# Kernel optimization log

Measured on AMD Instinct MI355X. Metric: run time of the kernel, lower is better.

The kernel has to match this reference:

```python
import jax, jax.numpy as jnp
import numpy as np

T = 8
TAU = 2.0       # spikingjelly LIFNode default tau
VTH = 1.0       # default v_threshold
ALPHA = 2.0     # surrogate.ATan alpha
EPS = 1e-5      # BatchNorm eps


@jax.custom_vjp
def spike_fn(x):
    # Heaviside with ATan surrogate gradient
    return (x >= 0.0).astype(x.dtype)

def _spike_fwd(x):
    return (x >= 0.0).astype(x.dtype), x

def _spike_bwd(x, g):
    sg = (ALPHA / 2.0) / (1.0 + (jnp.pi / 2.0 * ALPHA * x) ** 2)
    return (g * sg,)

spike_fn.defvjp(_spike_fwd, _spike_bwd)


def lif(x_seq):
    """Multi-step LIF over leading time axis. decay_input=True, hard reset to 0, detach_reset."""
    def step(v, x):
        v = v + (x - v) / TAU            # charge
        s = spike_fn(v - VTH)            # fire (surrogate grad)
        v = v * (1.0 - jax.lax.stop_gradient(s))  # detached hard reset to v_reset=0
        return v, s
    _, s_seq = jax.lax.scan(step, jnp.zeros_like(x_seq[0]), x_seq)
    return s_seq


def conv2d(x, w, b, stride):
    y = jax.lax.conv_general_dilated(x, w, (stride, stride), 'VALID',
                                     dimension_numbers=('NCHW', 'OIHW', 'NCHW'))
    return y + b[None, :, None, None]


def batchnorm(x, g, b):
    # training-mode BN over merged (T*B, H, W) axes, matching step_mode='m' BatchNorm2d
    m = x.mean((0, 2, 3), keepdims=True)
    v = x.var((0, 2, 3), keepdims=True)
    return g[None, :, None, None] * (x - m) * jax.lax.rsqrt(v + EPS) + b[None, :, None, None]


def setup_inputs() -> dict:
    key = jax.random.key(0)
    ks = jax.random.split(key, 12)
    def w_init(k, shape):
        fan_in = int(np.prod(shape[1:]))
        return jax.random.normal(k, shape, dtype=jnp.float32) / np.sqrt(fan_in)
    x = jax.random.normal(ks[0], (128, 4, 84, 84), dtype=jnp.float32)
    return {
        'x': x,
        'conv1_w': w_init(ks[1], (32, 4, 8, 8)),  'conv1_b': jnp.zeros((32,), jnp.float32),
        'bn1_g': jnp.ones((32,), jnp.float32),    'bn1_b': jnp.zeros((32,), jnp.float32),
        'conv2_w': w_init(ks[2], (64, 32, 4, 4)), 'conv2_b': jnp.zeros((64,), jnp.float32),
        'bn2_g': jnp.ones((64,), jnp.float32),    'bn2_b': jnp.zeros((64,), jnp.float32),
        'conv3_w': w_init(ks[3], (64, 64, 3, 3)), 'conv3_b': jnp.zeros((64,), jnp.float32),
        'bn3_g': jnp.ones((64,), jnp.float32),    'bn3_b': jnp.zeros((64,), jnp.float32),
        'fc1_w': w_init(ks[4], (512, 3136)),      'fc1_b': jnp.zeros((512,), jnp.float32),
        'fco_w': w_init(ks[5], (2, 512)),         'fco_b': jnp.zeros((2,), jnp.float32),
    }


def reference(x, conv1_w, conv1_b, bn1_g, bn1_b, conv2_w, conv2_b, bn2_g, bn2_b,
              conv3_w, conv3_b, bn3_g, bn3_b, fc1_w, fc1_b, fco_w, fco_b):
    B = x.shape[0]
    # replicate input over T timesteps; fold T into batch for conv/BN (step_mode='m')
    xs = jnp.broadcast_to(x, (T,) + x.shape).reshape((T * B,) + x.shape[1:])

    h = batchnorm(conv2d(xs, conv1_w, conv1_b, 4), bn1_g, bn1_b)   # [TB,32,20,20]
    s = lif(h.reshape((T, B) + h.shape[1:]))
    h = s.reshape((T * B,) + s.shape[2:])

    h = batchnorm(conv2d(h, conv2_w, conv2_b, 2), bn2_g, bn2_b)    # [TB,64,9,9]
    s = lif(h.reshape((T, B) + h.shape[1:]))
    h = s.reshape((T * B,) + s.shape[2:])

    h = batchnorm(conv2d(h, conv3_w, conv3_b, 1), bn3_g, bn3_b)    # [TB,64,7,7]
    s = lif(h.reshape((T, B) + h.shape[1:]))                        # [T,B,64,7,7]

    feat = s.reshape(T, B, -1)                                      # [T,B,3136]
    hid = lif(jnp.einsum('tbi,oi->tbo', feat, fc1_w) + fc1_b)       # [T,B,512]
    out_seq = jnp.einsum('tbo,ko->tbk', hid, fco_w) + fco_b         # [T,B,2]
    return out_seq.mean(0)                                          # [B,2]
```

## Files before the change

### kernel.cpp

```cpp
#include <hip/hip_runtime.h>
#include <cstdint>
#include <cstddef>

#define TT 8

#define E2_ELEMS (128*64*81)
#define E3_ELEMS (128*64*49)

typedef __attribute__((ext_vector_type(8))) short short8;
typedef __attribute__((ext_vector_type(4))) short short4v;
typedef __attribute__((ext_vector_type(4))) float f32x4;

#define BAR_LDS() do { asm volatile("s_waitcnt lgkmcnt(0)" ::: "memory"); \
                       __builtin_amdgcn_s_barrier(); } while (0)

__device__ __forceinline__ void gld_lds16(const void* g, void* l) {
  __builtin_amdgcn_global_load_lds((const __attribute__((address_space(1))) void*)g,
                                   (__attribute__((address_space(3))) void*)l, 16, 0, 0);
}

__device__ __forceinline__ void split3(float v, ushort& h, ushort& m, ushort& l) {
  union { __bf16 b; ushort u; } H, M, L;
  H.b = (__bf16)v; float r1 = v - (float)H.b;
  M.b = (__bf16)r1; float r2 = r1 - (float)M.b;
  L.b = (__bf16)r2;
  h = H.u; m = M.u; l = L.u;
}

__device__ __forceinline__ short8 ld8(const ushort* p) {
  union { short4v h[2]; short8 v; } U;
  U.h[0] = *(const short4v*)(p);
  U.h[1] = *(const short4v*)(p + 4);
  return U.v;
}

__global__ __launch_bounds__(256) void prep_all(const float* __restrict__ w1,
                                                const float* __restrict__ w2,
                                                const float* __restrict__ w3,
                                                const float* __restrict__ wfc,
                                                __bf16* __restrict__ w1f,
                                                __bf16* __restrict__ w2f,
                                                __bf16* __restrict__ w3f,
                                                __bf16* __restrict__ wff) {
  __shared__ float tile[12544];
  int bxx = blockIdx.x;
  int tid = threadIdx.x;

  if (bxx >= 912) {
    int bx2 = bxx - 912;
    int oc0 = (bx2 >> 3) * 32;
    int ci0 = (bx2 & 7) * 8;
    for (int f = tid; f < 12544; f += 256) {
      int oc_l = f / 392, r = f - oc_l * 392;
      tile[f] = wfc[(size_t)(oc0 + oc_l) * 3136 + ci0 * 49 + r];
    }
    __syncthreads();
    int squad = (ci0 & 31) >> 3;
    int sadd  = ci0 >> 5;
    for (int g = tid; g < 1568; g += 256) {
      int pos = g >> 5, oc_l = g & 31;
      union { __bf16 h[8]; uint4 u; } T0, T1, T2;
      #pragma unroll
      for (int j = 0; j < 8; j++) {
        float wv = tile[oc_l * 392 + j * 49 + pos];
        float hf = (float)(__bf16)wv;
        float r1 = wv - hf;
        float mf = (float)(__bf16)r1;
        float r2 = r1 - mf;
        T0.h[j] = (__bf16)wv; T1.h[j] = (__bf16)r1; T2.h[j] = (__bf16)r2;
      }
      int s = pos * 2 + sadd;
      size_t b0 = (((size_t)s * 4 + squad) * 512 + oc0 + oc_l) * 8;
      *(uint4*)(wff + b0)           = T0.u;
      *(uint4*)(wff + b0 + 1605632) = T1.u;
      *(uint4*)(wff + b0 + 3211264) = T2.u;
    }
    return;
  }

  int i = bxx * 256 + tid;
  if (i < 98304) {
    int v = i;
    int j    = v & 7;
    int oc   = (v >> 3) & 63;
    int quad = (v >> 9) & 3;
    int ksg  = (v >> 11) & 15;
    int term = v >> 15;
    int k = ksg * 32 + quad * 8 + j;
    int ci = k >> 4, kpos = k & 15;
    float w = w2[oc * 512 + ci * 16 + kpos];
    float hf = (float)(__bf16)w;
    float r1 = w - hf;
    float mf = (float)(__bf16)r1;
    float r2 = r1 - mf;
    w2f[v] = (term == 0) ? (__bf16)w : (term == 1) ? (__bf16)r1 : (__bf16)r2;
  } else if (i < 208896) {
    int v = i - 98304;
    int j    = v & 7;
    int oc   = (v >> 3) & 63;
    int quad = (v >> 9) & 3;
    int tk   = v >> 11;
    int term = tk / 18, kstep = tk % 18;
    int k = kstep * 32 + quad * 8 + j;
    int pos = k >> 6, ci = k & 63;
    float w = w3[oc * 576 + ci * 9 + pos];
    float hf = (float)(__bf16)w;
    float r1 = w - hf;
    float mf = (float)(__bf16)r1;
    float r2 = r1 - mf;
    w3f[v] = (term == 0) ? (__bf16)w : (term == 1) ? (__bf16)r1 : (__bf16)r2;
  } else {
    int v = i - 208896;
    int j    = v & 7;
    int oc   = (v >> 3) & 31;
    int quad = (v >> 8) & 3;
    int ks   = (v >> 10) & 7;
    int term = v >> 13;
    int k = ks * 32 + quad * 8 + j;
    float w = w1[oc * 256 + k];
    float hf = (float)(__bf16)w;
    float r1 = w - hf;
    float mf = (float)(__bf16)r1;
    float r2 = r1 - mf;
    w1f[v] = (term == 0) ? (__bf16)w : (term == 1) ? (__bf16)r1 : (__bf16)r2;
  }
}

__global__ __launch_bounds__(128) void k_conv1m(const float* __restrict__ x,
                                                const __bf16* __restrict__ w1f,
                                                const float* __restrict__ bias,
                                                float* __restrict__ out,
                                                float* __restrict__ pout) {
  __shared__ ushort xs[24192];
  int tid = threadIdx.x;
  int bx = blockIdx.x;
  int img = bx >> 2, q = bx & 3;
  const float* xb = x + (size_t)img * 28224 + q * 1680;
  for (int f = tid; f < 2016; f += 128) {
    int ci = f / 504, rr = f - ci * 504;
    int row = rr / 21, c4 = rr - row * 21;
    float4 v4 = *(const float4*)(xb + ci * 7056 + row * 84 + c4 * 4);
    union { ushort s[4]; uint2 u; } H, M, L;
    float vv[4] = {v4.x, v4.y, v4.z, v4.w};
    #pragma unroll
    for (int j = 0; j < 4; j++) split3(vv[j], H.s[j], M.s[j], L.s[j]);
    int eo = ci * 2016 + row * 84 + c4 * 4;
    *(uint2*)(xs + eo)         = H.u;
    *(uint2*)(xs + 8064 + eo)  = M.u;
    *(uint2*)(xs + 16128 + eo) = L.u;
  }
  __syncthreads();
  int nh = tid >> 6, lane = tid & 63;
  int l15 = lane & 15, quad = lane >> 4;
  int aoff[7];
  #pragma unroll
  for (int mt = 0; mt < 7; mt++) {
    int px = mt * 16 + l15; if (px > 99) px = 99;
    int oy = px / 20, ox = px - oy * 20;
    aoff[mt] = oy * 336 + ox * 4;
  }
  f32x4 acc[7];
  #pragma unroll
  for (int mt = 0; mt < 7; mt++) acc[mt] = (f32x4){0.f, 0.f, 0.f, 0.f};
  const __bf16* wpb = w1f + quad * 256 + (nh * 16 + l15) * 8;
  for (int ks = 0; ks < 8; ks++) {
    const __bf16* wp = wpb + ks * 1024;
    short8 bh = *(const short8*)(wp);
    short8 bm = *(const short8*)(wp + 8192);
    short8 bl = *(const short8*)(wp + 16384);
    int pair = ks * 4 + quad;
    int e0 = (pair >> 3) * 2016 + (pair & 7) * 84;
    short8 ah[7], am[7], al[7];
    #pragma unroll
    for (int mt = 0; mt < 7; mt++) {
      int e = e0 + aoff[mt];
      ah[mt] = ld8(xs + e);
      am[mt] = ld8(xs + 8064 + e);
      al[mt] = ld8(xs + 16128 + e);
    }
    #pragma unroll
    for (int mt = 0; mt < 7; mt++)
      acc[mt] = __builtin_amdgcn_mfma_f32_16x16x32_bf16(ah[mt], bh, acc[mt], 0, 0, 0);
    #pragma unroll
    for (int mt = 0; mt < 7; mt++)
      acc[mt] = __builtin_amdgcn_mfma_f32_16x16x32_bf16(ah[mt], bm, acc[mt], 0, 0, 0);
    #pragma unroll
    for (int mt = 0; mt < 7; mt++)
      acc[mt] = __builtin_amdgcn_mfma_f32_16x16x32_bf16(am[mt], bh, acc[mt], 0, 0, 0);
    #pragma unroll
    for (int mt = 0; mt < 7; mt++)
      acc[mt] = __builtin_amdgcn_mfma_f32_16x16x32_bf16(am[mt], bm, acc[mt], 0, 0, 0);
    #pragma unroll
    for (int mt = 0; mt < 7; mt++)
      acc[mt] = __builtin_amdgcn_mfma_f32_16x16x32_bf16(ah[mt], bl, acc[mt], 0, 0, 0);
    #pragma unroll
    for (int mt = 0; mt < 7; mt++)
      acc[mt] = __builtin_amdgcn_mfma_f32_16x16x32_bf16(al[mt], bh, acc[mt], 0, 0, 0);
    #pragma unroll
    for (int mt = 0; mt < 7; mt++)
      acc[mt] = __builtin_amdgcn_mfma_f32_16x16x32_bf16(am[mt], bl, acc[mt], 0, 0, 0);
    #pragma unroll
    for (int mt = 0; mt < 7; mt++)
      acc[mt] = __builtin_amdgcn_mfma_f32_16x16x32_bf16(al[mt], bm, acc[mt], 0, 0, 0);
  }
  int oc = nh * 16 + l15;
  float bv = bias[oc];
  float sl = 0.f, sl2 = 0.f;
  float* op = out + (size_t)img * 12800 + oc * 400 + q * 100;
  #pragma unroll
  for (int mt = 0; mt < 7; mt++) {
    int pxb = mt * 16 + quad * 4;
    #pragma unroll
    for (int r = 0; r < 4; r++) {
      int px = pxb + r;
      if (px < 100) {
        float v = acc[mt][r] + bv;
        op[px] = v;
        sl += v; sl2 += v * v;
      }
    }
  }
  __syncthreads();
  float* sred = (float*)xs;
  sred[oc * 4 + quad] = sl;
  sred[128 + oc * 4 + quad] = sl2;
  __syncthreads();
  if (tid < 32) {
    float s  = sred[tid*4] + sred[tid*4+1] + sred[tid*4+2] + sred[tid*4+3];
    float s2 = sred[128+tid*4] + sred[128+tid*4+1] + sred[128+tid*4+2] + sred[128+tid*4+3];
    pout[tid * 512 + bx] = s;
    pout[16384 + tid * 512 + bx] = s2;
  }
}

__global__ void k_bnfinal2(const float* __restrict__ pin, int sqoff, float n,
                           float* __restrict__ meanArr, float* __restrict__ rstdArr) {
  __shared__ float l0[256], l1[256];
  int c = blockIdx.x, tid = threadIdx.x;
  l0[tid] = pin[c * 512 + tid] + pin[c * 512 + tid + 256];
  l1[tid] = pin[sqoff + c * 512 + tid] + pin[sqoff + c * 512 + tid + 256];
  __syncthreads();
  for (int k = 128; k > 0; k >>= 1) {
    if (tid < k) { l0[tid] += l0[tid + k]; l1[tid] += l1[tid + k]; }
    __syncthreads();
  }
  if (tid == 0) {
    float m = l0[0] / n;
    float var = l1[0] / n - m * m;
    meanArr[c] = m;
    rstdArr[c] = rsqrtf(var + 1e-5f);
  }
}

__global__ void k_lif1b(const float* __restrict__ h, const float* __restrict__ mean,
                        const float* __restrict__ rstd, const float* __restrict__ g,
                        const float* __restrict__ bb, uint32_t* __restrict__ sout) {
  int idx = blockIdx.x * 256 + threadIdx.x;
  int ic = idx / 20;
  int ci = ic & 31;
  const float* hp = h + (size_t)idx * 20;
  float gm = g[ci], mm = mean[ci], rs = rstd[ci], bc = bb[ci];
  float xv[20];
  #pragma unroll
  for (int j4 = 0; j4 < 5; j4++) {
    float4 hv = ((const float4*)hp)[j4];
    xv[j4 * 4 + 0] = gm * (hv.x - mm) * rs + bc;
    xv[j4 * 4 + 1] = gm * (hv.y - mm) * rs + bc;
    xv[j4 * 4 + 2] = gm * (hv.z - mm) * rs + bc;
    xv[j4 * 4 + 3] = gm * (hv.w - mm) * rs + bc;
  }
  float v[20];
  #pragma unroll
  for (int j = 0; j < 20; j++) v[j] = 0.f;
  #pragma unroll
  for (int t = 0; t < TT; t++) {
    uint32_t w = 0;
    #pragma unroll
    for (int j = 0; j < 20; j++) {
      v[j] = v[j] + (xv[j] - v[j]) * 0.5f;
      uint32_t s = (v[j] >= 1.0f);
      w |= s << j;
      if (s) v[j] = 0.f;
    }
    sout[t * 81920 + idx] = w;
  }
}

__global__ __launch_bounds__(256) void k_conv2m(const uint32_t* __restrict__ s1b,
                                                const __bf16* __restrict__ wf,
                                                const float* __restrict__ bias,
                                                float* __restrict__ out,
                                                float* __restrict__ pout) {
  __shared__ uint32_t sp[1280];
  __shared__ uint4 wl4[3072];
  __bf16* wl = (__bf16*)wl4;
  int tid = threadIdx.x;
  int img0 = blockIdx.x * 2;
  {
    const uint32_t* src = s1b + (size_t)img0 * 640;
    for (int i = tid; i < 1280; i += 256) sp[i] = src[i];
  }
  int wave = tid >> 6, lane = tid & 63;
  int img_local = wave >> 1;
  int nh = wave & 1;
  int l15 = lane & 15, quad = lane >> 4;
  int ci_off = quad >> 1;
  int kyp = (quad & 1) * 2;
  int spb[6], sh[6];
  #pragma unroll
  for (int mt = 0; mt < 6; mt++) {
    int px = mt * 16 + l15;
    if (px > 80) px = 80;
    int oy = px / 9, ox = px - oy * 9;
    sh[mt]  = ox * 2;
    spb[mt] = img_local * 640 + ci_off * 20 + oy * 2 + kyp;
  }
  f32x4 acc[6][2];
  #pragma unroll
  for (int mt = 0; mt < 6; mt++)
    #pragma unroll
    for (int nt = 0; nt < 2; nt++) acc[mt][nt] = (f32x4){0.f, 0.f, 0.f, 0.f};

  for (int kc = 0; kc < 4; kc++) {
    __syncthreads();
    for (int o = tid * 8; o < 24576; o += 2048) {
      int tk = o >> 11;
      int term = tk >> 2, ksl = tk & 3;
      const __bf16* src = wf + (((term * 16 + kc * 4 + ksl)) << 11) + (o & 2047);
      gld_lds16(src, wl + o);
    }
    __syncthreads();
    #pragma unroll
    for (int ks = 0; ks < 4; ks++) {
      int ksg = kc * 4 + ks;
      short8 a[6];
      #pragma unroll
      for (int mt = 0; mt < 6; mt++) {
        uint32_t w0 = sp[spb[mt] + ksg * 40];
        uint32_t w1 = sp[spb[mt] + ksg * 40 + 1];
        uint32_t n0 = (w0 >> sh[mt]) & 15u;
        uint32_t n1 = (w1 >> sh[mt]) & 15u;
        union { uint32_t u[4]; short8 v; } A;
        A.u[0] = ((n0 & 1u) ? 0x3F80u : 0u) | ((n0 & 2u) ? 0x3F800000u : 0u);
        A.u[1] = ((n0 & 4u) ? 0x3F80u : 0u) | ((n0 & 8u) ? 0x3F800000u : 0u);
        A.u[2] = ((n1 & 1u) ? 0x3F80u : 0u) | ((n1 & 2u) ? 0x3F800000u : 0u);
        A.u[3] = ((n1 & 4u) ? 0x3F80u : 0u) | ((n1 & 8u) ? 0x3F800000u : 0u);
        a[mt] = A.v;
      }
      #pragma unroll
      for (int term = 0; term < 3; term++) {
        int fb = ((term * 4 + ks) << 11) + (quad << 9);
        #pragma unroll
        for (int nt = 0; nt < 2; nt++) {
          short8 b = *(const short8*)(wl + fb + ((((nh << 1) | nt) << 4) + l15) * 8);
          #pragma unroll
          for (int mt = 0; mt < 6; mt++)
            acc[mt][nt] = __builtin_amdgcn_mfma_f32_16x16x32_bf16(a[mt], b, acc[mt][nt], 0, 0, 0);
        }
      }
    }
  }
  float sl[2], sl2[2];
  #pragma unroll
  for (int nt = 0; nt < 2; nt++) {
    sl[nt] = 0.f; sl2[nt] = 0.f;
    int oc = nh * 32 + nt * 16 + l15;
    float bv = bias[oc];
    float* op = out + ((size_t)(img0 + img_local) * 64 + oc) * 81;
    #pragma unroll
    for (int mt = 0; mt < 6; mt++) {
      int pxr = mt * 16 + quad * 4;
      #pragma unroll
      for (int r = 0; r < 4; r++) {
        int px = pxr + r;
        if (px < 81) {
          float v = acc[mt][nt][r] + bv;
          op[px] = v;
          sl[nt] += v; sl2[nt] += v * v;
        }
      }
    }
  }
  __syncthreads();
  float* sred = (float*)wl4;
  #pragma unroll
  for (int nt = 0; nt < 2; nt++) {
    int oc = nh * 32 + nt * 16 + l15;
    int idx = oc * 8 + img_local * 4 + quad;
    sred[idx] = sl[nt];
    sred[512 + idx] = sl2[nt];
  }
  __syncthreads();
  if (tid < 64) {
    float s = 0.f, s2 = 0.f;
    #pragma unroll
    for (int k = 0; k < 8; k++) { s += sred[tid * 8 + k]; s2 += sred[512 + tid * 8 + k]; }
    pout[tid * 512 + blockIdx.x] = s;
    pout[32768 + tid * 512 + blockIdx.x] = s2;
  }
}

__global__ __launch_bounds__(256) void k_lifb2T(const float* __restrict__ h,
                                                const float* __restrict__ mean,
                                                const float* __restrict__ rstd,
                                                const float* __restrict__ g,
                                                const float* __restrict__ bb,
                                                uint32_t* __restrict__ s2T) {
  __shared__ uint32_t sb[288];
  int b = blockIdx.x, half = blockIdx.y;
  int tid = threadIdx.x;
  int c1 = half * 32 + tid / 9, py1 = tid % 9;
  bool has2 = tid < 32;
  int r2 = tid + 256;
  int c2i = half * 32 + r2 / 9, py2 = r2 % 9;
  float gm1 = g[c1], mm1 = mean[c1], rs1 = rstd[c1], bc1 = bb[c1];
  float gm2 = 0.f, mm2 = 0.f, rs2 = 0.f, bc2 = 0.f;
  if (has2) { gm2 = g[c2i]; mm2 = mean[c2i]; rs2 = rstd[c2i]; bc2 = bb[c2i]; }
  float v1[9], v2[9];
  #pragma unroll
  for (int j = 0; j < 9; j++) { v1[j] = 0.f; v2[j] = 0.f; }
  size_t base1 = ((size_t)b * 64 + c1) * 81 + py1 * 9;
  size_t base2 = has2 ? ((size_t)b * 64 + c2i) * 81 + py2 * 9 : base1;
  float c1v[9], c2v[9];
  {
    const float* hp = h;
    #pragma unroll
    for (int j = 0; j < 9; j++) c1v[j] = hp[base1 + j];
    if (has2) {
      #pragma unroll
      for (int j = 0; j < 9; j++) c2v[j] = hp[base2 + j];
    }
  }
  #pragma unroll 1
  for (int t = 0; t < TT; t++) {
    float n1v[9], n2v[9];
    if (t < TT - 1) {
      const float* hp = h + (size_t)(t + 1) * E2_ELEMS;
      #pragma unroll
      for (int j = 0; j < 9; j++) n1v[j] = hp[base1 + j];
      if (has2) {
        #pragma unroll
        for (int j = 0; j < 9; j++) n2v[j] = hp[base2 + j];
      }
    }
    uint32_t w = 0;
    #pragma unroll
    for (int j = 0; j < 9; j++) {
      float xv = gm1 * (c1v[j] - mm1) * rs1 + bc1;
      v1[j] = v1[j] + (xv - v1[j]) * 0.5f;
      uint32_t s = (v1[j] >= 1.0f);
      w |= s << j;
      if (s) v1[j] = 0.f;
    }
    sb[tid] = w;
    if (has2) {
      uint32_t w2 = 0;
      #pragma unroll
      for (int j = 0; j < 9; j++) {
        float xv = gm2 * (c2v[j] - mm2) * rs2 + bc2;
        v2[j] = v2[j] + (xv - v2[j]) * 0.5f;
        uint32_t s = (v2[j] >= 1.0f);
        w2 |= s << j;
        if (s) v2[j] = 0.f;
      }
      sb[r2] = w2;
    }
    BAR_LDS();
    if (tid < 81) {
      int r = tid / 9, cpix = tid - r * 9;
      uint32_t wo = 0;
      #pragma unroll
      for (int ci = 0; ci < 32; ci++)
        wo |= ((sb[ci * 9 + r] >> cpix) & 1u) << ci;
      s2T[(size_t)(t * 128 + b) * 162 + tid * 2 + half] = wo;
    }
    BAR_LDS();
    if (t < TT - 1) {
      #pragma unroll
      for (int j = 0; j < 9; j++) c1v[j] = n1v[j];
      if (has2) {
        #pragma unroll
        for (int j = 0; j < 9; j++) c2v[j] = n2v[j];
      }
    }
  }
}

__global__ __launch_bounds__(256) void k_conv3m(const uint32_t* __restrict__ s2T,
                                                const __bf16* __restrict__ wf,
                                                const float* __restrict__ bias,
                                                float* __restrict__ out,
                                                float* __restrict__ pout) {
  __shared__ uint32_t sp[324];
  __shared__ uint4 wl4[4608];
  __bf16* wl = (__bf16*)wl4;
  int tid = threadIdx.x;
  int img0 = blockIdx.x * 2;
  {
    const uint32_t* src = s2T + (size_t)img0 * 162;
    for (int i = tid; i < 324; i += 256) sp[i] = src[i];
  }
  int wave = tid >> 6, lane = tid & 63;
  int img_local = wave >> 1, nh = wave & 1;
  int l15 = lane & 15, quad = lane >> 4;
  int qsh = quad * 8;
  int base[4];
  #pragma unroll
  for (int mt = 0; mt < 4; mt++) {
    int px = mt * 16 + l15;
    if (px > 48) px = 48;
    int oy = px / 7, ox = px - oy * 7;
    base[mt] = img_local * 162 + (oy * 9 + ox) * 2;
  }
  f32x4 acc[4][2];
  #pragma unroll
  for (int mt = 0; mt < 4; mt++)
    #pragma unroll
    for (int nt = 0; nt < 2; nt++) acc[mt][nt] = (f32x4){0.f, 0.f, 0.f, 0.f};

  #pragma unroll
  for (int kc = 0; kc < 3; kc++) {
    __syncthreads();
    #pragma unroll
    for (int it = 0; it < 18; it++) {
      const __bf16* s = wf + (((it / 6) * 18 + kc * 6 + (it % 6)) << 11) + tid * 8;
      gld_lds16(s, wl + (it << 11) + tid * 8);
    }
    __syncthreads();
    #pragma unroll
    for (int ksl = 0; ksl < 6; ksl++) {
      int kstep = kc * 6 + ksl;
      int pos = kstep >> 1, cihalf = kstep & 1;
      int ky = pos / 3, kx = pos % 3;
      short8 a[4];
      #pragma unroll
      for (int mt = 0; mt < 4; mt++) {
        uint32_t word = sp[base[mt] + (ky * 9 + kx) * 2 + cihalf];
        uint32_t byt = (word >> qsh) & 255u;
        union { uint32_t u[4]; short8 v; } A;
        A.u[0] = ((byt & 1u)  ? 0x3F80u : 0u) | ((byt & 2u)   ? 0x3F800000u : 0u);
        A.u[1] = ((byt & 4u)  ? 0x3F80u : 0u) | ((byt & 8u)   ? 0x3F800000u : 0u);
        A.u[2] = ((byt & 16u) ? 0x3F80u : 0u) | ((byt & 32u)  ? 0x3F800000u : 0u);
        A.u[3] = ((byt & 64u) ? 0x3F80u : 0u) | ((byt & 128u) ? 0x3F800000u : 0u);
        a[mt] = A.v;
      }
      #pragma unroll
      for (int term = 0; term < 3; term++) {
        int fb = ((term * 6 + ksl) << 11) + (quad << 9);
        #pragma unroll
        for (int nt = 0; nt < 2; nt++) {
          short8 b = *(const short8*)(wl + fb + ((((nh << 1) | nt) << 4) + l15) * 8);
          #pragma unroll
          for (int mt = 0; mt < 4; mt++)
            acc[mt][nt] = __builtin_amdgcn_mfma_f32_16x16x32_bf16(a[mt], b, acc[mt][nt], 0, 0, 0);
        }
      }
    }
  }
  float sl[2], sl2[2];
  #pragma unroll
  for (int nt = 0; nt < 2; nt++) {
    sl[nt] = 0.f; sl2[nt] = 0.f;
    int oc = nh * 32 + nt * 16 + l15;
    float bv = bias[oc];
    float* op = out + ((size_t)(img0 + img_local) * 64 + oc) * 49;
    #pragma unroll
    for (int mt = 0; mt < 4; mt++) {
      int pxr = mt * 16 + quad * 4;
      #pragma unroll
      for (int r = 0; r < 4; r++) {
        int px = pxr + r;
        if (px < 49) {
          float v = acc[mt][nt][r] + bv;
          op[px] = v;
          sl[nt] += v; sl2[nt] += v * v;
        }
      }
    }
  }
  __syncthreads();
  float* sred = (float*)wl4;
  #pragma unroll
  for (int nt = 0; nt < 2; nt++) {
    int oc = nh * 32 + nt * 16 + l15;
    int idx = oc * 8 + img_local * 4 + quad;
    sred[idx] = sl[nt];
    sred[512 + idx] = sl2[nt];
  }
  __syncthreads();
  if (tid < 64) {
    float s = 0.f, s2 = 0.f;
    #pragma unroll
    for (int k = 0; k < 8; k++) { s += sred[tid * 8 + k]; s2 += sred[512 + tid * 8 + k]; }
    pout[tid * 512 + blockIdx.x] = s;
    pout[32768 + tid * 512 + blockIdx.x] = s2;
  }
}

__global__ __launch_bounds__(256) void k_lifb3T(const float* __restrict__ h,
                                                const float* __restrict__ mean,
                                                const float* __restrict__ rstd,
                                                const float* __restrict__ g,
                                                const float* __restrict__ bb,
                                                uint32_t* __restrict__ s3T) {
  __shared__ uint32_t sb[224];
  int b = blockIdx.x, half = blockIdx.y;
  int tid = threadIdx.x;
  bool active = tid < 224;
  int row = active ? tid : 0;
  int c = half * 32 + row / 7, py = row % 7;
  float gm = g[c], mm = mean[c], rs = rstd[c], bc = bb[c];
  float v[7];
  #pragma unroll
  for (int j = 0; j < 7; j++) v[j] = 0.f;
  size_t base = ((size_t)b * 64 + c) * 49 + py * 7;
  float cv[7];
  if (active) {
    #pragma unroll
    for (int j = 0; j < 7; j++) cv[j] = h[base + j];
  }
  #pragma unroll 1
  for (int t = 0; t < TT; t++) {
    float nv[7];
    if (active && t < TT - 1) {
      const float* hp = h + (size_t)(t + 1) * E3_ELEMS;
      #pragma unroll
      for (int j = 0; j < 7; j++) nv[j] = hp[base + j];
    }
    if (active) {
      uint32_t w = 0;
      #pragma unroll
      for (int j = 0; j < 7; j++) {
        float xv = gm * (cv[j] - mm) * rs + bc;
        v[j] = v[j] + (xv - v[j]) * 0.5f;
        uint32_t s = (v[j] >= 1.0f);
        w |= s << j;
        if (s) v[j] = 0.f;
      }
      sb[tid] = w;
    }
    BAR_LDS();
    if (tid < 49) {
      int py2 = tid / 7, px = tid - py2 * 7;
      uint32_t wo = 0;
      #pragma unroll
      for (int ci = 0; ci < 32; ci++)
        wo |= ((sb[ci * 7 + py2] >> px) & 1u) << ci;
      s3T[(size_t)(t * 128 + b) * 98 + tid * 2 + half] = wo;
    }
    BAR_LDS();
    if (active && t < TT - 1) {
      #pragma unroll
      for (int j = 0; j < 7; j++) cv[j] = nv[j];
    }
  }
}

__global__ __launch_bounds__(256) void k_fc1m(const uint32_t* __restrict__ s3T,
                                              const __bf16* __restrict__ wf,
                                              float* __restrict__ f1) {
  __shared__ uint32_t aS[6272];
  int tid = threadIdx.x;
  int row0 = blockIdx.x * 64;
  int oc0  = blockIdx.y * 16;
  {
    const uint32_t* src = s3T + (size_t)row0 * 98;
    for (int i = tid; i < 6272; i += 256) aS[i] = src[i];
  }
  __syncthreads();
  int wave = tid >> 6, lane = tid & 63;
  int l15 = lane & 15, quad = lane >> 4;
  int qsh = quad * 8;
  f32x4 acc[4];
  #pragma unroll
  for (int mt = 0; mt < 4; mt++) acc[mt] = (f32x4){0.f, 0.f, 0.f, 0.f};
  int nIter = (wave < 2) ? 25 : 24;
  #pragma unroll 2
  for (int i = 0; i < nIter; i++) {
    int ks = i * 4 + wave;
    short8 a[4];
    #pragma unroll
    for (int mt = 0; mt < 4; mt++) {
      uint32_t word = aS[(mt * 16 + l15) * 98 + ks];
      uint32_t byt = (word >> qsh) & 255u;
      union { uint32_t u[4]; short8 v; } A;
      A.u[0] = ((byt & 1u)  ? 0x3F80u : 0u) | ((byt & 2u)   ? 0x3F800000u : 0u);
      A.u[1] = ((byt & 4u)  ? 0x3F80u : 0u) | ((byt & 8u)   ? 0x3F800000u : 0u);
      A.u[2] = ((byt & 16u) ? 0x3F80u : 0u) | ((byt & 32u)  ? 0x3F800000u : 0u);
      A.u[3] = ((byt & 64u) ? 0x3F80u : 0u) | ((byt & 128u) ? 0x3F800000u : 0u);
      a[mt] = A.v;
    }
    #pragma unroll
    for (int term = 0; term < 3; term++) {
      size_t fb = ((size_t)((term * 98 + ks) * 4 + quad) * 512 + oc0 + l15) * 8;
      short8 b = *(const short8*)(wf + fb);
      #pragma unroll
      for (int mt = 0; mt < 4; mt++)
        acc[mt] = __builtin_amdgcn_mfma_f32_16x16x32_bf16(a[mt], b, acc[mt], 0, 0, 0);
    }
  }
  __syncthreads();
  float* red = (float*)aS;
  #pragma unroll
  for (int mt = 0; mt < 4; mt++)
    #pragma unroll
    for (int r = 0; r < 4; r++)
      red[(wave * 64 + lane) * 17 + mt * 4 + r] = acc[mt][r];
  __syncthreads();
  #pragma unroll
  for (int k = 0; k < 4; k++) {
    int oi = tid + k * 256;
    int row_l = oi >> 4, oc_l = oi & 15;
    int mt = row_l >> 4, rem = row_l & 15;
    int q2 = rem >> 2, r = rem & 3;
    int ln = q2 * 16 + oc_l;
    float s = red[(0 * 64 + ln) * 17 + mt * 4 + r];
    s += red[(1 * 64 + ln) * 17 + mt * 4 + r];
    s += red[(2 * 64 + ln) * 17 + mt * 4 + r];
    s += red[(3 * 64 + ln) * 17 + mt * 4 + r];
    f1[(size_t)(row0 + row_l) * 512 + oc0 + oc_l] = s;
  }
}

__global__ __launch_bounds__(256) void k_fc1fco(const float* __restrict__ f1,
                                                const float* __restrict__ bias,
                                                const float* __restrict__ w,
                                                const float* __restrict__ fcob,
                                                float* __restrict__ out) {
  int b = blockIdx.x, tid = threadIdx.x;
  int o0 = tid, o1 = tid + 256;
  float bv0 = bias[o0], bv1 = bias[o1];
  float w00 = w[o0], w10 = w[512 + o0];
  float w01 = w[o1], w11 = w[512 + o1];
  float x0[TT], x1[TT];
  #pragma unroll
  for (int t = 0; t < TT; t++) {
    x0[t] = f1[(size_t)(t * 128 + b) * 512 + o0];
    x1[t] = f1[(size_t)(t * 128 + b) * 512 + o1];
  }
  float v0 = 0.f, v1 = 0.f;
  float a0 = 0.f, a1 = 0.f;
  #pragma unroll
  for (int t = 0; t < TT; t++) {
    float s0 = x0[t] + bv0;
    v0 = v0 + (s0 - v0) * 0.5f;
    bool sp0 = (v0 >= 1.0f);
    if (sp0) v0 = 0.f;
    float s1 = x1[t] + bv1;
    v1 = v1 + (s1 - v1) * 0.5f;
    bool sp1 = (v1 >= 1.0f);
    if (sp1) v1 = 0.f;
    if (sp0) { a0 += w00; a1 += w10; }
    if (sp1) { a0 += w01; a1 += w11; }
  }
  __shared__ float l0[256], l1[256];
  l0[tid] = a0; l1[tid] = a1; __syncthreads();
  for (int k = 128; k > 0; k >>= 1) {
    if (tid < k) { l0[tid] += l0[tid + k]; l1[tid] += l1[tid + k]; }
    __syncthreads();
  }
  if (tid == 0) {
    out[b * 2 + 0] = l0[0] * 0.125f + fcob[0];
    out[b * 2 + 1] = l1[0] * 0.125f + fcob[1];
  }
}

extern "C" void kernel_launch(void* const* d_in, const int* in_sizes, int n_in,
                              void* d_out, int out_size, void* d_ws, size_t ws_size,
                              hipStream_t stream) {
  const float* x    = (const float*)d_in[0];
  const float* c1w  = (const float*)d_in[1];
  const float* c1b  = (const float*)d_in[2];
  const float* bn1g = (const float*)d_in[3];
  const float* bn1b = (const float*)d_in[4];
  const float* c2w  = (const float*)d_in[5];
  const float* c2b  = (const float*)d_in[6];
  const float* bn2g = (const float*)d_in[7];
  const float* bn2b = (const float*)d_in[8];
  const float* c3w  = (const float*)d_in[9];
  const float* c3b  = (const float*)d_in[10];
  const float* bn3g = (const float*)d_in[11];
  const float* bn3b = (const float*)d_in[12];
  const float* fc1w = (const float*)d_in[13];
  const float* fc1b = (const float*)d_in[14];
  const float* fcow = (const float*)d_in[15];
  const float* fcob = (const float*)d_in[16];
  float* out = (float*)d_out;

  char* ws = (char*)d_ws;
  float*    h1     = (float*)(ws + 0);
  uint32_t* s1bits = (uint32_t*)(ws + 6553600);
  float*    h2     = (float*)(ws + 19660800);
  float*    h3     = (float*)(ws + 46202880);
  __bf16*   w2f    = (__bf16*)(ws + 60882944);
  __bf16*   w3f    = (__bf16*)(ws + 61079552);
  uint32_t* s2T    = (uint32_t*)(ws + 61300736);
  __bf16*   w1f    = (__bf16*)(ws + 62390272);
  float*    st     = (float*)(ws + 64880640);
  __bf16*   wff    = (__bf16*)(ws + 67108864);
  float*    f1sum  = (float*)(ws + 76742656);
  uint32_t* s3T    = (uint32_t*)(ws + 85131264);
  float*    bnpart = (float*)(ws + 85532672);

  prep_all   <<<1040, 256, 0, stream>>>(c1w, c2w, c3w, fc1w, w1f, w2f, w3f, wff);

  k_conv1m   <<<512, 128, 0, stream>>>(x, w1f, c1b, h1, bnpart);
  k_bnfinal2 <<<32, 256, 0, stream>>>(bnpart, 16384, 51200.f, st, st + 32);
  k_lif1b    <<<320, 256, 0, stream>>>(h1, st, st + 32, bn1g, bn1b, s1bits);

  k_conv2m   <<<512, 256, 0, stream>>>(s1bits, w2f, c2b, h2, bnpart);
  k_bnfinal2 <<<64, 256, 0, stream>>>(bnpart, 32768, 82944.f, st + 64, st + 128);
  k_lifb2T   <<<dim3(128, 2), 256, 0, stream>>>(h2, st + 64, st + 128, bn2g, bn2b, s2T);

  k_conv3m   <<<512, 256, 0, stream>>>(s2T, w3f, c3b, h3, bnpart);
  k_bnfinal2 <<<64, 256, 0, stream>>>(bnpart, 32768, 50176.f, st + 192, st + 256);
  k_lifb3T   <<<dim3(128, 2), 256, 0, stream>>>(h3, st + 192, st + 256, bn3g, bn3b, s3T);

  k_fc1m     <<<dim3(16, 32), 256, 0, stream>>>(s3T, wff, f1sum);
  k_fc1fco   <<<128, 256, 0, stream>>>(f1sum, fc1b, fcow, fcob, out);
}
```

Baseline: 233.0 us.

## Fuse BN finalization into consumers and LIF1 into conv2 input staging

Removes the three k_bnfinal2 launches: each consumer block now reduces the BN partial sums itself with wave shuffles and keeps mean/rstd in shared memory. It also removes k_lif1b and the s1bits buffer. conv2 recomputes layer-1 BN+LIF spike bits for its images directly from h1, re-running the LIF recurrence up to the block's timestep. This cuts kernel launches and one global round trip. The cost is redundant work: every block repeats the stats reduction, and the LIF recurrence is recomputed per timestep, up to 8 iterations with a data-dependent loop.

```diff
diff --git a/kernel.cpp b/kernel.cpp
--- a/kernel.cpp
+++ b/kernel.cpp
@@ -32,6 +32,34 @@
   U.h[0] = *(const short4v*)(p);
   U.h[1] = *(const short4v*)(p + 4);
   return U.v;
+}
+
+__device__ __forceinline__ void bn_wave_stats(const float* __restrict__ p0,
+                                              const float* __restrict__ p1,
+                                              int ln, float n,
+                                              float* __restrict__ stm,
+                                              float* __restrict__ str, int cl) {
+  float a0 = p0[ln]       + p0[ln + 256];
+  float a2 = p0[ln + 128] + p0[ln + 384];
+  float a1 = p0[ln + 64]  + p0[ln + 320];
+  float a3 = p0[ln + 192] + p0[ln + 448];
+  float s  = (a0 + a2) + (a1 + a3);
+  float q0 = p1[ln]       + p1[ln + 256];
+  float q2 = p1[ln + 128] + p1[ln + 384];
+  float q1 = p1[ln + 64]  + p1[ln + 320];
+  float q3 = p1[ln + 192] + p1[ln + 448];
+  float sq = (q0 + q2) + (q1 + q3);
+  #pragma unroll
+  for (int mask = 32; mask >= 1; mask >>= 1) {
+    s  += __shfl_xor(s,  mask);
+    sq += __shfl_xor(sq, mask);
+  }
+  if (ln == 0) {
+    float m = s / n;
+    float var = sq / n - m * m;
+    stm[cl] = m;
+    str[cl] = rsqrtf(var + 1e-5f);
+  }
 }
 
 __global__ __launch_bounds__(256) void prep_all(const float* __restrict__ w1,
@@ -233,73 +261,52 @@
   }
 }
 
-__global__ void k_bnfinal2(const float* __restrict__ pin, int sqoff, float n,
-                           float* __restrict__ meanArr, float* __restrict__ rstdArr) {
-  __shared__ float l0[256], l1[256];
-  int c = blockIdx.x, tid = threadIdx.x;
-  l0[tid] = pin[c * 512 + tid] + pin[c * 512 + tid + 256];
-  l1[tid] = pin[sqoff + c * 512 + tid] + pin[sqoff + c * 512 + tid + 256];
-  __syncthreads();
-  for (int k = 128; k > 0; k >>= 1) {
-    if (tid < k) { l0[tid] += l0[tid + k]; l1[tid] += l1[tid + k]; }
-    __syncthreads();
-  }
-  if (tid == 0) {
-    float m = l0[0] / n;
-    float var = l1[0] / n - m * m;
-    meanArr[c] = m;
-    rstdArr[c] = rsqrtf(var + 1e-5f);
-  }
-}
-
-__global__ void k_lif1b(const float* __restrict__ h, const float* __restrict__ mean,
-                        const float* __restrict__ rstd, const float* __restrict__ g,
-                        const float* __restrict__ bb, uint32_t* __restrict__ sout) {
-  int idx = blockIdx.x * 256 + threadIdx.x;
-  int ic = idx / 20;
-  int ci = ic & 31;
-  const float* hp = h + (size_t)idx * 20;
-  float gm = g[ci], mm = mean[ci], rs = rstd[ci], bc = bb[ci];
-  float xv[20];
-  #pragma unroll
-  for (int j4 = 0; j4 < 5; j4++) {
-    float4 hv = ((const float4*)hp)[j4];
-    xv[j4 * 4 + 0] = gm * (hv.x - mm) * rs + bc;
-    xv[j4 * 4 + 1] = gm * (hv.y - mm) * rs + bc;
-    xv[j4 * 4 + 2] = gm * (hv.z - mm) * rs + bc;
-    xv[j4 * 4 + 3] = gm * (hv.w - mm) * rs + bc;
-  }
-  float v[20];
-  #pragma unroll
-  for (int j = 0; j < 20; j++) v[j] = 0.f;
-  #pragma unroll
-  for (int t = 0; t < TT; t++) {
-    uint32_t w = 0;
-    #pragma unroll
-    for (int j = 0; j < 20; j++) {
-      v[j] = v[j] + (xv[j] - v[j]) * 0.5f;
-      uint32_t s = (v[j] >= 1.0f);
-      w |= s << j;
-      if (s) v[j] = 0.f;
-    }
-    sout[t * 81920 + idx] = w;
-  }
-}
-
-__global__ __launch_bounds__(256) void k_conv2m(const uint32_t* __restrict__ s1b,
+__global__ __launch_bounds__(256) void k_conv2m(const float* __restrict__ h1,
+                                                const float* __restrict__ bnp,
+                                                const float* __restrict__ g1,
+                                                const float* __restrict__ b1,
                                                 const __bf16* __restrict__ wf,
                                                 const float* __restrict__ bias,
                                                 float* __restrict__ out,
                                                 float* __restrict__ pout) {
   __shared__ uint32_t sp[1280];
   __shared__ uint4 wl4[3072];
+  __shared__ float stm[32], str[32];
   __bf16* wl = (__bf16*)wl4;
   int tid = threadIdx.x;
   int img0 = blockIdx.x * 2;
-  {
-    const uint32_t* src = s1b + (size_t)img0 * 640;
-    for (int i = tid; i < 1280; i += 256) sp[i] = src[i];
-  }
+  int t_blk = img0 >> 7;
+  int b0 = img0 & 127;
+  int wavei = tid >> 6, ln = tid & 63;
+  for (int c = wavei; c < 32; c += 4)
+    bn_wave_stats(bnp + c * 512, bnp + 16384 + c * 512, ln, 51200.f, stm, str, c);
+  __syncthreads();
+  for (int wi = tid; wi < 1280; wi += 256) {
+    int img_local = wi / 640, r = wi - img_local * 640;
+    int ci = (r / 20) & 31;
+    const float* hp = h1 + ((size_t)(b0 + img_local) * 640 + r) * 20;
+    float gm = g1[ci], mm = stm[ci], rs = str[ci], bc = b1[ci];
+    uint32_t w = 0;
+    #pragma unroll
+    for (int j4 = 0; j4 < 5; j4++) {
+      float4 hv = ((const float4*)hp)[j4];
+      float xsv[4] = {hv.x, hv.y, hv.z, hv.w};
+      #pragma unroll
+      for (int j = 0; j < 4; j++) {
+        float xv = gm * (xsv[j] - mm) * rs + bc;
+        float v = 0.f; uint32_t sbit = 0;
+        for (int tt = 0; tt <= t_blk; tt++) {
+          v = v + (xv - v) * 0.5f;
+          sbit = (v >= 1.0f);
+          if (sbit) v = 0.f;
+        }
+        w |= sbit << (j4 * 4 + j);
+      }
+    }
+    sp[wi] = w;
+  }
+  __syncthreads();
+
   int wave = tid >> 6, lane = tid & 63;
   int img_local = wave >> 1;
   int nh = wave & 1;
@@ -401,21 +408,27 @@
 }
 
 __global__ __launch_bounds__(256) void k_lifb2T(const float* __restrict__ h,
-                                                const float* __restrict__ mean,
-                                                const float* __restrict__ rstd,
+                                                const float* __restrict__ bnp,
                                                 const float* __restrict__ g,
                                                 const float* __restrict__ bb,
                                                 uint32_t* __restrict__ s2T) {
   __shared__ uint32_t sb[288];
+  __shared__ float stm[32], str[32];
   int b = blockIdx.x, half = blockIdx.y;
   int tid = threadIdx.x;
+  int wavei = tid >> 6, ln = tid & 63;
+  for (int cl = wavei; cl < 32; cl += 4) {
+    int c = half * 32 + cl;
+    bn_wave_stats(bnp + c * 512, bnp + 32768 + c * 512, ln, 82944.f, stm, str, cl);
+  }
+  __syncthreads();
   int c1 = half * 32 + tid / 9, py1 = tid % 9;
   bool has2 = tid < 32;
   int r2 = tid + 256;
   int c2i = half * 32 + r2 / 9, py2 = r2 % 9;
-  float gm1 = g[c1], mm1 = mean[c1], rs1 = rstd[c1], bc1 = bb[c1];
+  float gm1 = g[c1], mm1 = stm[tid / 9], rs1 = str[tid / 9], bc1 = bb[c1];
   float gm2 = 0.f, mm2 = 0.f, rs2 = 0.f, bc2 = 0.f;
-  if (has2) { gm2 = g[c2i]; mm2 = mean[c2i]; rs2 = rstd[c2i]; bc2 = bb[c2i]; }
+  if (has2) { gm2 = g[c2i]; mm2 = stm[r2 / 9]; rs2 = str[r2 / 9]; bc2 = bb[c2i]; }
   float v1[9], v2[9];
   #pragma unroll
   for (int j = 0; j < 9; j++) { v1[j] = 0.f; v2[j] = 0.f; }
@@ -598,18 +611,24 @@
 }
 
 __global__ __launch_bounds__(256) void k_lifb3T(const float* __restrict__ h,
-                                                const float* __restrict__ mean,
-                                                const float* __restrict__ rstd,
+                                                const float* __restrict__ bnp,
                                                 const float* __restrict__ g,
                                                 const float* __restrict__ bb,
                                                 uint32_t* __restrict__ s3T) {
   __shared__ uint32_t sb[224];
+  __shared__ float stm[32], str[32];
   int b = blockIdx.x, half = blockIdx.y;
   int tid = threadIdx.x;
+  int wavei = tid >> 6, ln = tid & 63;
+  for (int cl = wavei; cl < 32; cl += 4) {
+    int c = half * 32 + cl;
+    bn_wave_stats(bnp + c * 512, bnp + 32768 + c * 512, ln, 50176.f, stm, str, cl);
+  }
+  __syncthreads();
   bool active = tid < 224;
   int row = active ? tid : 0;
   int c = half * 32 + row / 7, py = row % 7;
-  float gm = g[c], mm = mean[c], rs = rstd[c], bc = bb[c];
+  float gm = g[c], mm = stm[row / 7], rs = str[row / 7], bc = bb[c];
   float v[7];
   #pragma unroll
   for (int j = 0; j < 7; j++) v[j] = 0.f;
@@ -789,33 +808,27 @@
 
   char* ws = (char*)d_ws;
   float*    h1     = (float*)(ws + 0);
-  uint32_t* s1bits = (uint32_t*)(ws + 6553600);
   float*    h2     = (float*)(ws + 19660800);
   float*    h3     = (float*)(ws + 46202880);
   __bf16*   w2f    = (__bf16*)(ws + 60882944);
   __bf16*   w3f    = (__bf16*)(ws + 61079552);
   uint32_t* s2T    = (uint32_t*)(ws + 61300736);
   __bf16*   w1f    = (__bf16*)(ws + 62390272);
-  float*    st     = (float*)(ws + 64880640);
   __bf16*   wff    = (__bf16*)(ws + 67108864);
   float*    f1sum  = (float*)(ws + 76742656);
   uint32_t* s3T    = (uint32_t*)(ws + 85131264);
-  float*    bnpart = (float*)(ws + 85532672);
-
-  prep_all   <<<1040, 256, 0, stream>>>(c1w, c2w, c3w, fc1w, w1f, w2f, w3f, wff);
-
-  k_conv1m   <<<512, 128, 0, stream>>>(x, w1f, c1b, h1, bnpart);
-  k_bnfinal2 <<<32, 256, 0, stream>>>(bnpart, 16384, 51200.f, st, st + 32);
-  k_lif1b    <<<320, 256, 0, stream>>>(h1, st, st + 32, bn1g, bn1b, s1bits);
-
-  k_conv2m   <<<512, 256, 0, stream>>>(s1bits, w2f, c2b, h2, bnpart);
-  k_bnfinal2 <<<64, 256, 0, stream>>>(bnpart, 32768, 82944.f, st + 64, st + 128);
-  k_lifb2T   <<<dim3(128, 2), 256, 0, stream>>>(h2, st + 64, st + 128, bn2g, bn2b, s2T);
-
-  k_conv3m   <<<512, 256, 0, stream>>>(s2T, w3f, c3b, h3, bnpart);
-  k_bnfinal2 <<<64, 256, 0, stream>>>(bnpart, 32768, 50176.f, st + 192, st + 256);
-  k_lifb3T   <<<dim3(128, 2), 256, 0, stream>>>(h3, st + 192, st + 256, bn3g, bn3b, s3T);
-
-  k_fc1m     <<<dim3(16, 32), 256, 0, stream>>>(s3T, wff, f1sum);
-  k_fc1fco   <<<128, 256, 0, stream>>>(f1sum, fc1b, fcow, fcob, out);
-}
+  float*    bnpA   = (float*)(ws + 85532672);
+  float*    bnpB   = (float*)(ws + 85794816);
+
+  prep_all <<<1040, 256, 0, stream>>>(c1w, c2w, c3w, fc1w, w1f, w2f, w3f, wff);
+
+  k_conv1m <<<512, 128, 0, stream>>>(x, w1f, c1b, h1, bnpA);
+  k_conv2m <<<512, 256, 0, stream>>>(h1, bnpA, bn1g, bn1b, w2f, c2b, h2, bnpB);
+  k_lifb2T <<<dim3(128, 2), 256, 0, stream>>>(h2, bnpB, bn2g, bn2b, s2T);
+
+  k_conv3m <<<512, 256, 0, stream>>>(s2T, w3f, c3b, h3, bnpB);
+  k_lifb3T <<<dim3(128, 2), 256, 0, stream>>>(h3, bnpB, bn3g, bn3b, s3T);
+
+  k_fc1m   <<<dim3(16, 32), 256, 0, stream>>>(s3T, wff, f1sum);
+  k_fc1fco <<<128, 256, 0, stream>>>(f1sum, fc1b, fcow, fcob, out);
+}
```

Measured after the change: 262.6 us. 1.13x slower.

## Split conv2/conv3 blocks by output-channel half and preload full weight slice

Applied to the files above, without the earlier changes.

Conv2 and conv3 blocks now each handle four images and one half of the output channels, instead of two images and all channels. Each block loads its whole weight slice into LDS once before the main loop, so the per-chunk reload and barriers inside the K loop go away. The partial-stat reduction is reindexed so the per-512 pout layout stays the same. LDS use per block grows a lot (about 100-115 KB), which may cut occupancy to one block per CU. The staged weight load is no longer overlapped with compute.

```diff
diff --git a/kernel.cpp b/kernel.cpp
--- a/kernel.cpp
+++ b/kernel.cpp
@@ -291,18 +291,31 @@
                                                 const float* __restrict__ bias,
                                                 float* __restrict__ out,
                                                 float* __restrict__ pout) {
-  __shared__ uint32_t sp[1280];
-  __shared__ uint4 wl4[3072];
+  __shared__ uint4 wl4[6144];
+  __shared__ uint32_t sp[2560];
+  __shared__ float sred[1024];
   __bf16* wl = (__bf16*)wl4;
   int tid = threadIdx.x;
-  int img0 = blockIdx.x * 2;
+  int bx = blockIdx.x;
+  int img_group = bx >> 1;
+  int nh = bx & 1;
   {
-    const uint32_t* src = s1b + (size_t)img0 * 640;
-    for (int i = tid; i < 1280; i += 256) sp[i] = src[i];
-  }
+    const uint32_t* src = s1b + (size_t)img_group * 2560;
+    for (int i = tid; i < 2560; i += 256) sp[i] = src[i];
+  }
+  #pragma unroll
+  for (int r = 0; r < 24; r++) {
+    int idx = r * 256 + tid;
+    int chunk = idx >> 5, ln32 = idx & 31;
+    int quad_c = chunk & 3, tq = chunk >> 2;
+    int term = tq % 3, ksg = tq / 3;
+    const __bf16* src = wf + term * 32768 + ksg * 2048 + quad_c * 512 + nh * 256 + ln32 * 8;
+    gld_lds16(src, wl + idx * 8);
+  }
+  __syncthreads();
+
   int wave = tid >> 6, lane = tid & 63;
-  int img_local = wave >> 1;
-  int nh = wave & 1;
+  int img = img_group * 4 + wave;
   int l15 = lane & 15, quad = lane >> 4;
   int ci_off = quad >> 1;
   int kyp = (quad & 1) * 2;
@@ -313,7 +326,7 @@
     if (px > 80) px = 80;
     int oy = px / 9, ox = px - oy * 9;
     sh[mt]  = ox * 2;
-    spb[mt] = img_local * 640 + ci_off * 20 + oy * 2 + kyp;
+    spb[mt] = wave * 640 + ci_off * 20 + oy * 2 + kyp;
   }
   f32x4 acc[6][2];
   #pragma unroll
@@ -321,42 +334,30 @@
     #pragma unroll
     for (int nt = 0; nt < 2; nt++) acc[mt][nt] = (f32x4){0.f, 0.f, 0.f, 0.f};
 
-  for (int kc = 0; kc < 4; kc++) {
-    __syncthreads();
-    for (int o = tid * 8; o < 24576; o += 2048) {
-      int tk = o >> 11;
-      int term = tk >> 2, ksl = tk & 3;
-      const __bf16* src = wf + (((term * 16 + kc * 4 + ksl)) << 11) + (o & 2047);
-      gld_lds16(src, wl + o);
-    }
-    __syncthreads();
-    #pragma unroll
-    for (int ks = 0; ks < 4; ks++) {
-      int ksg = kc * 4 + ks;
-      short8 a[6];
-      #pragma unroll
-      for (int mt = 0; mt < 6; mt++) {
-        uint32_t w0 = sp[spb[mt] + ksg * 40];
-        uint32_t w1 = sp[spb[mt] + ksg * 40 + 1];
-        uint32_t n0 = (w0 >> sh[mt]) & 15u;
-        uint32_t n1 = (w1 >> sh[mt]) & 15u;
-        union { uint32_t u[4]; short8 v; } A;
-        A.u[0] = ((n0 & 1u) ? 0x3F80u : 0u) | ((n0 & 2u) ? 0x3F800000u : 0u);
-        A.u[1] = ((n0 & 4u) ? 0x3F80u : 0u) | ((n0 & 8u) ? 0x3F800000u : 0u);
-        A.u[2] = ((n1 & 1u) ? 0x3F80u : 0u) | ((n1 & 2u) ? 0x3F800000u : 0u);
-        A.u[3] = ((n1 & 4u) ? 0x3F80u : 0u) | ((n1 & 8u) ? 0x3F800000u : 0u);
-        a[mt] = A.v;
-      }
-      #pragma unroll
-      for (int term = 0; term < 3; term++) {
-        int fb = ((term * 4 + ks) << 11) + (quad << 9);
+  #pragma unroll 2
+  for (int ksg = 0; ksg < 16; ksg++) {
+    short8 a[6];
+    #pragma unroll
+    for (int mt = 0; mt < 6; mt++) {
+      uint32_t w0 = sp[spb[mt] + ksg * 40];
+      uint32_t w1 = sp[spb[mt] + ksg * 40 + 1];
+      uint32_t n0 = (w0 >> sh[mt]) & 15u;
+      uint32_t n1 = (w1 >> sh[mt]) & 15u;
+      union { uint32_t u[4]; short8 v; } A;
+      A.u[0] = ((n0 & 1u) ? 0x3F80u : 0u) | ((n0 & 2u) ? 0x3F800000u : 0u);
+      A.u[1] = ((n0 & 4u) ? 0x3F80u : 0u) | ((n0 & 8u) ? 0x3F800000u : 0u);
+      A.u[2] = ((n1 & 1u) ? 0x3F80u : 0u) | ((n1 & 2u) ? 0x3F800000u : 0u);
+      A.u[3] = ((n1 & 4u) ? 0x3F80u : 0u) | ((n1 & 8u) ? 0x3F800000u : 0u);
+      a[mt] = A.v;
+    }
+    #pragma unroll
+    for (int term = 0; term < 3; term++) {
+      #pragma unroll
+      for (int nt = 0; nt < 2; nt++) {
+        short8 b = *(const short8*)(wl + (((ksg * 3 + term) * 4 + quad) << 8) + (nt * 16 + l15) * 8);
         #pragma unroll
-        for (int nt = 0; nt < 2; nt++) {
-          short8 b = *(const short8*)(wl + fb + ((((nh << 1) | nt) << 4) + l15) * 8);
-          #pragma unroll
-          for (int mt = 0; mt < 6; mt++)
-            acc[mt][nt] = __builtin_amdgcn_mfma_f32_16x16x32_bf16(a[mt], b, acc[mt][nt], 0, 0, 0);
-        }
+        for (int mt = 0; mt < 6; mt++)
+          acc[mt][nt] = __builtin_amdgcn_mfma_f32_16x16x32_bf16(a[mt], b, acc[mt][nt], 0, 0, 0);
       }
     }
   }
@@ -364,9 +365,10 @@
   #pragma unroll
   for (int nt = 0; nt < 2; nt++) {
     sl[nt] = 0.f; sl2[nt] = 0.f;
-    int oc = nh * 32 + nt * 16 + l15;
+    int ocl = nt * 16 + l15;
+    int oc = nh * 32 + ocl;
     float bv = bias[oc];
-    float* op = out + ((size_t)(img0 + img_local) * 64 + oc) * 81;
+    float* op = out + ((size_t)img * 64 + oc) * 81;
     #pragma unroll
     for (int mt = 0; mt < 6; mt++) {
       int pxr = mt * 16 + quad * 4;
@@ -382,21 +384,23 @@
     }
   }
   __syncthreads();
-  float* sred = (float*)wl4;
   #pragma unroll
   for (int nt = 0; nt < 2; nt++) {
-    int oc = nh * 32 + nt * 16 + l15;
-    int idx = oc * 8 + img_local * 4 + quad;
-    sred[idx] = sl[nt];
-    sred[512 + idx] = sl2[nt];
+    int ocl = nt * 16 + l15;
+    sred[ocl * 16 + wave * 4 + quad] = sl[nt];
+    sred[512 + ocl * 16 + wave * 4 + quad] = sl2[nt];
   }
   __syncthreads();
   if (tid < 64) {
+    int ocl = tid >> 1, bxl = tid & 1;
     float s = 0.f, s2 = 0.f;
     #pragma unroll
-    for (int k = 0; k < 8; k++) { s += sred[tid * 8 + k]; s2 += sred[512 + tid * 8 + k]; }
-    pout[tid * 512 + blockIdx.x] = s;
-    pout[32768 + tid * 512 + blockIdx.x] = s2;
+    for (int k = 0; k < 8; k++) {
+      s  += sred[ocl * 16 + bxl * 8 + k];
+      s2 += sred[512 + ocl * 16 + bxl * 8 + k];
+    }
+    pout[(nh * 32 + ocl) * 512 + img_group * 2 + bxl] = s;
+    pout[32768 + (nh * 32 + ocl) * 512 + img_group * 2 + bxl] = s2;
   }
 }
 
@@ -491,17 +495,31 @@
                                                 const float* __restrict__ bias,
                                                 float* __restrict__ out,
                                                 float* __restrict__ pout) {
-  __shared__ uint32_t sp[324];
-  __shared__ uint4 wl4[4608];
+  __shared__ uint4 wl4[6912];
+  __shared__ uint32_t sp[648];
+  __shared__ float sred[1024];
   __bf16* wl = (__bf16*)wl4;
   int tid = threadIdx.x;
-  int img0 = blockIdx.x * 2;
+  int bx = blockIdx.x;
+  int img_group = bx >> 1;
+  int nh = bx & 1;
   {
-    const uint32_t* src = s2T + (size_t)img0 * 162;
-    for (int i = tid; i < 324; i += 256) sp[i] = src[i];
-  }
+    const uint32_t* src = s2T + (size_t)img_group * 648;
+    for (int i = tid; i < 648; i += 256) sp[i] = src[i];
+  }
+  #pragma unroll
+  for (int r = 0; r < 27; r++) {
+    int idx = r * 256 + tid;
+    int chunk = idx >> 5, ln32 = idx & 31;
+    int quad_c = chunk & 3, tq = chunk >> 2;
+    int term = tq % 3, kstep = tq / 3;
+    const __bf16* src = wf + (term * 18 + kstep) * 2048 + quad_c * 512 + nh * 256 + ln32 * 8;
+    gld_lds16(src, wl + idx * 8);
+  }
+  __syncthreads();
+
   int wave = tid >> 6, lane = tid & 63;
-  int img_local = wave >> 1, nh = wave & 1;
+  int img = img_group * 4 + wave;
   int l15 = lane & 15, quad = lane >> 4;
   int qsh = quad * 8;
   int base[4];
@@ -510,7 +528,7 @@
     int px = mt * 16 + l15;
     if (px > 48) px = 48;
     int oy = px / 7, ox = px - oy * 7;
-    base[mt] = img_local * 162 + (oy * 9 + ox) * 2;
+    base[mt] = wave * 162 + (oy * 9 + ox) * 2;
   }
   f32x4 acc[4][2];
   #pragma unroll
@@ -518,42 +536,30 @@
     #pragma unroll
     for (int nt = 0; nt < 2; nt++) acc[mt][nt] = (f32x4){0.f, 0.f, 0.f, 0.f};
 
-  #pragma unroll
-  for (int kc = 0; kc < 3; kc++) {
-    __syncthreads();
-    #pragma unroll
-    for (int it = 0; it < 18; it++) {
-      const __bf16* s = wf + (((it / 6) * 18 + kc * 6 + (it % 6)) << 11) + tid * 8;
-      gld_lds16(s, wl + (it << 11) + tid * 8);
-    }
-    __syncthreads();
-    #pragma unroll
-    for (int ksl = 0; ksl < 6; ksl++) {
-      int kstep = kc * 6 + ksl;
-      int pos = kstep >> 1, cihalf = kstep & 1;
-      int ky = pos / 3, kx = pos % 3;
-      short8 a[4];
-      #pragma unroll
-      for (int mt = 0; mt < 4; mt++) {
-        uint32_t word = sp[base[mt] + (ky * 9 + kx) * 2 + cihalf];
-        uint32_t byt = (word >> qsh) & 255u;
-        union { uint32_t u[4]; short8 v; } A;
-        A.u[0] = ((byt & 1u)  ? 0x3F80u : 0u) | ((byt & 2u)   ? 0x3F800000u : 0u);
-        A.u[1] = ((byt & 4u)  ? 0x3F80u : 0u) | ((byt & 8u)   ? 0x3F800000u : 0u);
-        A.u[2] = ((byt & 16u) ? 0x3F80u : 0u) | ((byt & 32u)  ? 0x3F800000u : 0u);
-        A.u[3] = ((byt & 64u) ? 0x3F80u : 0u) | ((byt & 128u) ? 0x3F800000u : 0u);
-        a[mt] = A.v;
-      }
-      #pragma unroll
-      for (int term = 0; term < 3; term++) {
-        int fb = ((term * 6 + ksl) << 11) + (quad << 9);
+  #pragma unroll 2
+  for (int kstep = 0; kstep < 18; kstep++) {
+    int pos = kstep >> 1, cihalf = kstep & 1;
+    int ky = pos / 3, kx = pos % 3;
+    short8 a[4];
+    #pragma unroll
+    for (int mt = 0; mt < 4; mt++) {
+      uint32_t word = sp[base[mt] + (ky * 9 + kx) * 2 + cihalf];
+      uint32_t byt = (word >> qsh) & 255u;
+      union { uint32_t u[4]; short8 v; } A;
+      A.u[0] = ((byt & 1u)  ? 0x3F80u : 0u) | ((byt & 2u)   ? 0x3F800000u : 0u);
+      A.u[1] = ((byt & 4u)  ? 0x3F80u : 0u) | ((byt & 8u)   ? 0x3F800000u : 0u);
+      A.u[2] = ((byt & 16u) ? 0x3F80u : 0u) | ((byt & 32u)  ? 0x3F800000u : 0u);
+      A.u[3] = ((byt & 64u) ? 0x3F80u : 0u) | ((byt & 128u) ? 0x3F800000u : 0u);
+      a[mt] = A.v;
+    }
+    #pragma unroll
+    for (int term = 0; term < 3; term++) {
+      #pragma unroll
+      for (int nt = 0; nt < 2; nt++) {
+        short8 b = *(const short8*)(wl + (((kstep * 3 + term) * 4 + quad) << 8) + (nt * 16 + l15) * 8);
         #pragma unroll
-        for (int nt = 0; nt < 2; nt++) {
-          short8 b = *(const short8*)(wl + fb + ((((nh << 1) | nt) << 4) + l15) * 8);
-          #pragma unroll
-          for (int mt = 0; mt < 4; mt++)
-            acc[mt][nt] = __builtin_amdgcn_mfma_f32_16x16x32_bf16(a[mt], b, acc[mt][nt], 0, 0, 0);
-        }
+        for (int mt = 0; mt < 4; mt++)
+          acc[mt][nt] = __builtin_amdgcn_mfma_f32_16x16x32_bf16(a[mt], b, acc[mt][nt], 0, 0, 0);
       }
     }
   }
@@ -561,9 +567,10 @@
   #pragma unroll
   for (int nt = 0; nt < 2; nt++) {
     sl[nt] = 0.f; sl2[nt] = 0.f;
-    int oc = nh * 32 + nt * 16 + l15;
+    int ocl = nt * 16 + l15;
+    int oc = nh * 32 + ocl;
     float bv = bias[oc];
-    float* op = out + ((size_t)(img0 + img_local) * 64 + oc) * 49;
+    float* op = out + ((size_t)img * 64 + oc) * 49;
     #pragma unroll
     for (int mt = 0; mt < 4; mt++) {
       int pxr = mt * 16 + quad * 4;
@@ -579,21 +586,23 @@
     }
   }
   __syncthreads();
-  float* sred = (float*)wl4;
   #pragma unroll
   for (int nt = 0; nt < 2; nt++) {
-    int oc = nh * 32 + nt * 16 + l15;
-    int idx = oc * 8 + img_local * 4 + quad;
-    sred[idx] = sl[nt];
-    sred[512 + idx] = sl2[nt];
+    int ocl = nt * 16 + l15;
+    sred[ocl * 16 + wave * 4 + quad] = sl[nt];
+    sred[512 + ocl * 16 + wave * 4 + quad] = sl2[nt];
   }
   __syncthreads();
   if (tid < 64) {
+    int ocl = tid >> 1, bxl = tid & 1;
     float s = 0.f, s2 = 0.f;
     #pragma unroll
-    for (int k = 0; k < 8; k++) { s += sred[tid * 8 + k]; s2 += sred[512 + tid * 8 + k]; }
-    pout[tid * 512 + blockIdx.x] = s;
-    pout[32768 + tid * 512 + blockIdx.x] = s2;
+    for (int k = 0; k < 8; k++) {
+      s  += sred[ocl * 16 + bxl * 8 + k];
+      s2 += sred[512 + ocl * 16 + bxl * 8 + k];
+    }
+    pout[(nh * 32 + ocl) * 512 + img_group * 2 + bxl] = s;
+    pout[32768 + (nh * 32 + ocl) * 512 + img_group * 2 + bxl] = s2;
   }
 }
 
```

After: 243.8 us. +4.7%, slower.
